# Optimization experiments

Hardware: AMD Instinct MI355X
Metric: run time of the kernel (lower is better)

## Reference

```python
import jax, jax.numpy as jnp
import numpy as np

B = 4096        # num_graphs
N = 524288      # total nodes per node type
D_IN = 128
D_OUT = 256     # embedding_out_shape (hard-coded in module)


def _make_ptr(key, n, b):
    inner = jnp.sort(jax.random.randint(key, (b - 1,), 0, n + 1)).astype(jnp.int32)
    return jnp.concatenate([jnp.zeros(1, jnp.int32), inner, jnp.full((1,), n, jnp.int32)])


def setup_inputs() -> dict:
    key = jax.random.key(0)
    ks = jax.random.split(key, 8)
    s = 1.0 / np.sqrt(D_IN)
    return {
        "x_a": jax.random.normal(ks[0], (N, D_IN), jnp.float32),
        "W_a": jax.random.uniform(ks[1], (D_IN, D_OUT), jnp.float32, -s, s),
        "b_a": jax.random.uniform(ks[2], (D_OUT,), jnp.float32, -s, s),
        "x_b": jax.random.normal(ks[3], (N, D_IN), jnp.float32),
        "W_b": jax.random.uniform(ks[4], (D_IN, D_OUT), jnp.float32, -s, s),
        "b_b": jax.random.uniform(ks[5], (D_OUT,), jnp.float32, -s, s),
        "ptr_a": _make_ptr(ks[6], N, B),
        "ptr_b": _make_ptr(ks[7], N, B),
    }


def _segment_mean_from_ptr(y, ptr, num_graphs):
    # node i belongs to graph g s.t. ptr[g] <= i < ptr[g+1]
    n = y.shape[0]
    seg = jnp.searchsorted(ptr, jnp.arange(n, dtype=ptr.dtype), side='right') - 1
    sums = jax.ops.segment_sum(y, seg, num_segments=num_graphs)  # [B, D_OUT]
    counts = (ptr[1:] - ptr[:-1]).astype(y.dtype)                # [B]
    # empty graphs keep zero rows (sums are 0; divide by 1)
    return sums / jnp.maximum(counts, 1)[:, None]


def reference(x_a, W_a, b_a, x_b, W_b, b_b, ptr_a, ptr_b):
    y_a = x_a @ W_a + b_a  # set encoder for node type a
    y_b = x_b @ W_b + b_b  # set encoder for node type b
    e_a = _segment_mean_from_ptr(y_a, ptr_a, B)
    e_b = _segment_mean_from_ptr(y_b, ptr_b, B)
    return jnp.concatenate([e_a, e_b], axis=1)  # [B, 2*D_OUT]
```

## Files before the change

### kernel.cpp

```cpp
#include <hip/hip_runtime.h>
#include <stdint.h>

#define NGRAPHS 4096
#define DIN 128
#define DOUT 256

__global__ __launch_bounds__(256)
void seg_encode_kernel(const float* __restrict__ x_a, const float* __restrict__ W_a,
                       const float* __restrict__ b_a, const int* __restrict__ ptr_a,
                       const float* __restrict__ x_b, const float* __restrict__ W_b,
                       const float* __restrict__ b_b, const int* __restrict__ ptr_b,
                       float* __restrict__ out) {
    const int g   = blockIdx.x;
    const int t   = blockIdx.y;
    const int tid = threadIdx.x;

    const float* __restrict__ x    = t ? x_b  : x_a;
    const float* __restrict__ W    = t ? W_b  : W_a;
    const float* __restrict__ bias = t ? b_b  : b_a;
    const int*   __restrict__ ptr  = t ? ptr_b : ptr_a;

    const int s = ptr[g];
    const int e = ptr[g + 1];
    const int n = e - s;

    float* __restrict__ orow = out + (size_t)g * (2 * DOUT) + t * DOUT;

    if (n == 0) {
        orow[tid] = 0.0f;
        return;
    }

    __shared__ float red[8][DIN];
    __shared__ float mean[DIN];

    const int slot = tid & 31;
    const int r    = tid >> 5;

    float4 acc = make_float4(0.f, 0.f, 0.f, 0.f);

    const float* __restrict__ xs = x + (size_t)slot * 4;
    for (int i = s + r; i < e; i += 8) {
        float4 v = *(const float4*)(xs + (size_t)i * DIN);
        acc.x += v.x; acc.y += v.y; acc.z += v.z; acc.w += v.w;
    }

    red[r][slot * 4 + 0] = acc.x;
    red[r][slot * 4 + 1] = acc.y;
    red[r][slot * 4 + 2] = acc.z;
    red[r][slot * 4 + 3] = acc.w;
    __syncthreads();

    if (tid < DIN) {
        float sum = 0.0f;
#pragma unroll
        for (int rr = 0; rr < 8; ++rr) sum += red[rr][tid];
        mean[tid] = sum * (1.0f / (float)n);
    }
    __syncthreads();

    float o = bias[tid];
    const float* __restrict__ wcol = W + tid;
#pragma unroll 8
    for (int k = 0; k < DIN; ++k) {
        o += mean[k] * wcol[(size_t)k * DOUT];
    }
    orow[tid] = o;
}

extern "C" void kernel_launch(void* const* d_in, const int* in_sizes, int n_in,
                              void* d_out, int out_size, void* d_ws, size_t ws_size,
                              hipStream_t stream) {
    const float* x_a  = (const float*)d_in[0];
    const float* W_a  = (const float*)d_in[1];
    const float* b_a  = (const float*)d_in[2];
    const float* x_b  = (const float*)d_in[3];
    const float* W_b  = (const float*)d_in[4];
    const float* b_b  = (const float*)d_in[5];
    const int*   ptr_a = (const int*)d_in[6];
    const int*   ptr_b = (const int*)d_in[7];
    float* out = (float*)d_out;

    dim3 grid(NGRAPHS, 2);
    seg_encode_kernel<<<grid, 256, 0, stream>>>(x_a, W_a, b_a, ptr_a,
                                                x_b, W_b, b_b, ptr_b, out);
}
```

Baseline: 579.9 us.

## Split into node-tiled segment sum with atomics and batched per-graph matmul

Result: faster. 545.6 us (-5.9%).

```diff
diff --git a/kernel.cpp b/kernel.cpp
--- a/kernel.cpp
+++ b/kernel.cpp
@@ -2,15 +2,138 @@
 #include <stdint.h>
 
 #define NGRAPHS 4096
-#define DIN 128
-#define DOUT 256
+#define NNODES  524288
+#define DIN     128
+#define DOUT    256
+#define TILE    512
+#define G2      8
+
 
 __global__ __launch_bounds__(256)
-void seg_encode_kernel(const float* __restrict__ x_a, const float* __restrict__ W_a,
-                       const float* __restrict__ b_a, const int* __restrict__ ptr_a,
-                       const float* __restrict__ x_b, const float* __restrict__ W_b,
-                       const float* __restrict__ b_b, const int* __restrict__ ptr_b,
-                       float* __restrict__ out) {
+void zero_ws(float4* __restrict__ ws) {
+    ws[(size_t)blockIdx.x * 256 + threadIdx.x] = make_float4(0.f, 0.f, 0.f, 0.f);
+}
+
+__global__ __launch_bounds__(256, 8)
+void seg_sum_kernel(const float* __restrict__ x_a, const int* __restrict__ ptr_a,
+                    const float* __restrict__ x_b, const int* __restrict__ ptr_b,
+                    float* __restrict__ sums) {
+    const int t = blockIdx.y;
+    const float* __restrict__ x   = t ? x_b  : x_a;
+    const int*   __restrict__ ptr = t ? ptr_b : ptr_a;
+    float* __restrict__ seg = sums + (size_t)t * NGRAPHS * DIN;
+
+    const int r0 = blockIdx.x * TILE;
+    const int r1 = r0 + TILE;
+
+    const int tid  = threadIdx.x;
+    const int slot = tid & 31;
+    const int r    = tid >> 5;
+
+    __shared__ float red[8][DIN];
+
+    int lo = 0, hi = NGRAPHS;
+    while (lo < hi) {
+        int mid = (lo + hi) >> 1;
+        if (ptr[mid] <= r0) lo = mid + 1; else hi = mid;
+    }
+    int g = lo - 1;
+
+    const float* __restrict__ xs = x + (size_t)slot * 4;
+
+    for (;;) {
+        const int ss = ptr[g];
+        const int ee = ptr[g + 1];
+        const int a  = ss > r0 ? ss : r0;
+        const int b  = ee < r1 ? ee : r1;
+
+        if (b > a) {
+            float4 acc = make_float4(0.f, 0.f, 0.f, 0.f);
+            for (int i = a + r; i < b; i += 8) {
+                const float4 v = *(const float4*)(xs + (size_t)i * DIN);
+                acc.x += v.x; acc.y += v.y; acc.z += v.z; acc.w += v.w;
+            }
+            red[r][slot * 4 + 0] = acc.x;
+            red[r][slot * 4 + 1] = acc.y;
+            red[r][slot * 4 + 2] = acc.z;
+            red[r][slot * 4 + 3] = acc.w;
+            __syncthreads();
+            if (tid < DIN) {
+                float v = 0.f;
+#pragma unroll
+                for (int rr = 0; rr < 8; ++rr) v += red[rr][tid];
+                float* dst = seg + (size_t)g * DIN + tid;
+                if (ss >= r0 && ee <= r1) *dst = v;
+                else                      atomicAdd(dst, v);
+            }
+            __syncthreads();
+        }
+        if (ee >= r1) break;
+        ++g;
+    }
+}
+
+__global__ __launch_bounds__(256)
+void seg_mm_kernel(const float* __restrict__ W_a, const float* __restrict__ b_a,
+                   const int* __restrict__ ptr_a,
+                   const float* __restrict__ W_b, const float* __restrict__ b_b,
+                   const int* __restrict__ ptr_b,
+                   const float* __restrict__ sums, float* __restrict__ out) {
+    const int t = blockIdx.y;
+    const float* __restrict__ W    = t ? W_b  : W_a;
+    const float* __restrict__ bias = t ? b_b  : b_a;
+    const int*   __restrict__ ptr  = t ? ptr_b : ptr_a;
+    const float* __restrict__ seg  = sums + (size_t)t * NGRAPHS * DIN;
+
+    const int g0  = blockIdx.x * G2;
+    const int tid = threadIdx.x;
+
+    __shared__ __align__(16) float mean[G2][DIN];
+    __shared__ float cnt[G2];
+
+    if (tid < G2) {
+        int n = ptr[g0 + tid + 1] - ptr[g0 + tid];
+        cnt[tid] = (float)(n > 0 ? n : 1);
+    }
+    __syncthreads();
+    for (int idx = tid; idx < G2 * DIN; idx += 256) {
+        int gg = idx >> 7, k = idx & 127;
+        mean[gg][k] = seg[(size_t)(g0 + gg) * DIN + k] / cnt[gg];
+    }
+    __syncthreads();
+
+    float acc[G2];
+#pragma unroll
+    for (int gg = 0; gg < G2; ++gg) acc[gg] = 0.f;
+
+    const float* __restrict__ wcol = W + tid;
+    for (int k = 0; k < DIN; k += 4) {
+        float w0 = wcol[(size_t)(k + 0) * DOUT];
+        float w1 = wcol[(size_t)(k + 1) * DOUT];
+        float w2 = wcol[(size_t)(k + 2) * DOUT];
+        float w3 = wcol[(size_t)(k + 3) * DOUT];
+#pragma unroll
+        for (int gg = 0; gg < G2; ++gg) {
+            const float4 m = *(const float4*)&mean[gg][k];
+            acc[gg] += m.x * w0 + m.y * w1 + m.z * w2 + m.w * w3;
+        }
+    }
+
+    const float bv = bias[tid];
+#pragma unroll
+    for (int gg = 0; gg < G2; ++gg) {
+        const int g = g0 + gg;
+        const int n = ptr[g + 1] - ptr[g];
+        out[(size_t)g * (2 * DOUT) + t * DOUT + tid] = (n > 0) ? acc[gg] + bv : 0.f;
+    }
+}
+
+__global__ __launch_bounds__(256)
+void seg_encode_fallback(const float* __restrict__ x_a, const float* __restrict__ W_a,
+                         const float* __restrict__ b_a, const int* __restrict__ ptr_a,
+                         const float* __restrict__ x_b, const float* __restrict__ W_b,
+                         const float* __restrict__ b_b, const int* __restrict__ ptr_b,
+                         float* __restrict__ out) {
     const int g   = blockIdx.x;
     const int t   = blockIdx.y;
     const int tid = threadIdx.x;
@@ -25,32 +148,24 @@
     const int n = e - s;
 
     float* __restrict__ orow = out + (size_t)g * (2 * DOUT) + t * DOUT;
-
-    if (n == 0) {
-        orow[tid] = 0.0f;
-        return;
-    }
+    if (n == 0) { orow[tid] = 0.0f; return; }
 
     __shared__ float red[8][DIN];
     __shared__ float mean[DIN];
 
     const int slot = tid & 31;
     const int r    = tid >> 5;
-
     float4 acc = make_float4(0.f, 0.f, 0.f, 0.f);
-
     const float* __restrict__ xs = x + (size_t)slot * 4;
     for (int i = s + r; i < e; i += 8) {
         float4 v = *(const float4*)(xs + (size_t)i * DIN);
         acc.x += v.x; acc.y += v.y; acc.z += v.z; acc.w += v.w;
     }
-
     red[r][slot * 4 + 0] = acc.x;
     red[r][slot * 4 + 1] = acc.y;
     red[r][slot * 4 + 2] = acc.z;
     red[r][slot * 4 + 3] = acc.w;
     __syncthreads();
-
     if (tid < DIN) {
         float sum = 0.0f;
 #pragma unroll
@@ -58,13 +173,10 @@
         mean[tid] = sum * (1.0f / (float)n);
     }
     __syncthreads();
-
     float o = bias[tid];
     const float* __restrict__ wcol = W + tid;
 #pragma unroll 8
-    for (int k = 0; k < DIN; ++k) {
-        o += mean[k] * wcol[(size_t)k * DOUT];
-    }
+    for (int k = 0; k < DIN; ++k) o += mean[k] * wcol[(size_t)k * DOUT];
     orow[tid] = o;
 }
 
@@ -81,7 +193,23 @@
     const int*   ptr_b = (const int*)d_in[7];
     float* out = (float*)d_out;
 
-    dim3 grid(NGRAPHS, 2);
-    seg_encode_kernel<<<grid, 256, 0, stream>>>(x_a, W_a, b_a, ptr_a,
-                                                x_b, W_b, b_b, ptr_b, out);
-}
+    const size_t ws_needed = (size_t)2 * NGRAPHS * DIN * sizeof(float);
+
+    if (d_ws == nullptr || ws_size < ws_needed) {
+        dim3 grid(NGRAPHS, 2);
+        seg_encode_fallback<<<grid, 256, 0, stream>>>(x_a, W_a, b_a, ptr_a,
+                                                      x_b, W_b, b_b, ptr_b, out);
+        return;
+    }
+
+    float* sums = (float*)d_ws;
+
+    zero_ws<<<(2 * NGRAPHS * DIN) / (256 * 4), 256, 0, stream>>>((float4*)sums);
+
+    dim3 grid1(NNODES / TILE, 2);
+    seg_sum_kernel<<<grid1, 256, 0, stream>>>(x_a, ptr_a, x_b, ptr_b, sums);
+
+    dim3 grid2(NGRAPHS / G2, 2);
+    seg_mm_kernel<<<grid2, 256, 0, stream>>>(W_a, b_a, ptr_a, W_b, b_b, ptr_b,
+                                             sums, out);
+}
```
